# Kernel tuning notes

Measured on AMD Instinct MI355X. Metric: run time of the kernel, lower is better.

The kernel has to match this reference:

```python
import jax, jax.numpy as jnp
import numpy as np

JITTER = 1e-6
LOG_2PI_BASE = 2.0 * np.pi  # multiplied by sigma_sq inside log


def rbf_kernel(x1, x2, lengthscale, outputscale):
    """gpytorch ScaleKernel(RBFKernel): outputscale * exp(-0.5 * ||(x1-x2)/ls||^2)."""
    x1s = x1 / lengthscale
    x2s = x2 / lengthscale
    sq = (jnp.sum(x1s * x1s, axis=1)[:, None]
          + jnp.sum(x2s * x2s, axis=1)[None, :]
          - 2.0 * (x1s @ x2s.T))
    sq = jnp.maximum(sq, 0.0)
    return outputscale * jnp.exp(-0.5 * sq)


def setup_inputs() -> dict:
    key = jax.random.key(0)
    k = jax.random.split(key, 4)
    n, m, d = 8192, 512, 8
    return {
        "train_x": jax.random.normal(k[0], (n, d), dtype=jnp.float32),
        "train_y": jax.random.normal(k[1], (n,), dtype=jnp.float32),
        "inducing_points": jax.random.normal(k[2], (m, d), dtype=jnp.float32),
        "q_mu": jnp.zeros((m, 1), dtype=jnp.float32),
        "q_log_var": jnp.eye(m, dtype=jnp.float32),
        "likelihood_log_variance": jnp.asarray(0.0, dtype=jnp.float32),
        "lengthscale": jnp.asarray(1.0, dtype=jnp.float32),
        "outputscale": jnp.asarray(1.0, dtype=jnp.float32),
    }


def reference(train_x, train_y, inducing_points, q_mu, q_log_var,
              likelihood_log_variance, lengthscale, outputscale):
    n = train_x.shape[0]
    m = inducing_points.shape[0]
    eye_m = jnp.eye(m, dtype=train_x.dtype)

    # --- predict(train_x): q(f) = N(pred_mean, pred_cov) ---
    K_ff = rbf_kernel(train_x, train_x, lengthscale, outputscale)          # [n, n]
    K_uu = rbf_kernel(inducing_points, inducing_points, lengthscale, outputscale) + JITTER * eye_m
    K_uf = rbf_kernel(inducing_points, train_x, lengthscale, outputscale)  # [m, n]

    L_uu = jnp.linalg.cholesky(K_uu)                                       # lower [m, m]
    Lam = jax.scipy.linalg.solve_triangular(L_uu, K_uf, lower=True)        # [m, n]
    pred_mean = (Lam.T @ q_mu)[:, 0]                                       # [n]

    q_sqrt = jnp.tril(jnp.exp(0.5 * q_log_var))                            # [m, m]
    q_cov = q_sqrt @ q_sqrt.T + JITTER * eye_m                             # [m, m]

    S = K_ff - Lam.T @ Lam                                                 # [n, n]
    V = Lam.T @ q_cov                                                      # [n, m]
    pred_cov = S + V @ V.T                                                 # [n, n]

    # --- expected log likelihood E_{q(f)}[log N(y | f, sigma^2 I)] / n ---
    sigma_sq = jnp.exp(likelihood_log_variance)
    diff = train_y - pred_mean
    ell = jnp.sum(-0.5 * (diff * diff + jnp.diagonal(pred_cov)) / sigma_sq
                  - 0.5 * jnp.log(LOG_2PI_BASE * sigma_sq)) / n

    # --- KL( N(q_mu, q_cov) || N(0, I) ) / n ---
    Lq = jnp.linalg.cholesky(q_cov)
    logdet_q = 2.0 * jnp.sum(jnp.log(jnp.diagonal(Lq)))
    mu = q_mu[:, 0]
    kl = 0.5 * (jnp.trace(q_cov) + mu @ mu - m - logdet_q) / n

    return ell - kl
```

## Files before the change

### kernel.cpp

```cpp
#include <hip/hip_runtime.h>
#include <math.h>

#define MI 512
#define NPT 8192
#define JIT 1e-6f
#define LOG2PI 1.8378770664093453f

#define OFF_A     0
#define OFF_LINV  262144
#define OFF_QS    524288
#define OFF_QC    786432
#define OFF_DINV  1048576
#define OFF_PART  1081856
#define OFF_FLAGS 1082368
#define NFLAGS 211

#define FMA16(ACC,a0,a1,a2,a3,b0,b1,b2,b3) \
  ACC[0][0]+=a0*b0; ACC[0][1]+=a0*b1; ACC[0][2]+=a0*b2; ACC[0][3]+=a0*b3; \
  ACC[1][0]+=a1*b0; ACC[1][1]+=a1*b1; ACC[1][2]+=a1*b2; ACC[1][3]+=a1*b3; \
  ACC[2][0]+=a2*b0; ACC[2][1]+=a2*b1; ACC[2][2]+=a2*b2; ACC[2][3]+=a2*b3; \
  ACC[3][0]+=a3*b0; ACC[3][1]+=a3*b1; ACC[3][2]+=a3*b2; ACC[3][3]+=a3*b3;

typedef float f4 __attribute__((ext_vector_type(4)));

__device__ __forceinline__ f4 ld_coh(const float* p) {
  f4 r;
  asm volatile("global_load_dwordx4 %0, %1, off sc0 sc1\n\ts_waitcnt vmcnt(0)"
               : "=v"(r) : "v"(p) : "memory");
  return r;
}
__device__ __forceinline__ void ld_coh4x4(const float* p0, const float* p1,
    const float* p2, const float* p3, f4& a, f4& b, f4& c, f4& d) {
  asm volatile(
    "global_load_dwordx4 %0, %4, off sc0 sc1\n\t"
    "global_load_dwordx4 %1, %5, off sc0 sc1\n\t"
    "global_load_dwordx4 %2, %6, off sc0 sc1\n\t"
    "global_load_dwordx4 %3, %7, off sc0 sc1\n\t"
    "s_waitcnt vmcnt(0)"
    : "=&v"(a), "=&v"(b), "=&v"(c), "=&v"(d)
    : "v"(p0), "v"(p1), "v"(p2), "v"(p3) : "memory");
}
__device__ __forceinline__ void st_coh(float* p, f4 v) {
  asm volatile("global_store_dwordx4 %0, %1, off sc0 sc1" :: "v"(p), "v"(v) : "memory");
}

__device__ __forceinline__ void wait_flag(unsigned* f, int tid) {
  if (tid == 0) {
    while (__hip_atomic_load(f, __ATOMIC_RELAXED, __HIP_MEMORY_SCOPE_AGENT) == 0)
      __builtin_amdgcn_s_sleep(2);
    __builtin_amdgcn_fence(__ATOMIC_ACQUIRE, "agent");
  }
  __syncthreads();
}
__device__ __forceinline__ void wait_count(unsigned* c, unsigned tgt, int tid) {
  if (tid == 0) {
    while (__hip_atomic_load(c, __ATOMIC_RELAXED, __HIP_MEMORY_SCOPE_AGENT) < tgt)
      __builtin_amdgcn_s_sleep(2);
    __builtin_amdgcn_fence(__ATOMIC_ACQUIRE, "agent");
  }
  __syncthreads();
}
__device__ __forceinline__ void publish_tile(unsigned* f, unsigned* cnt, int tid) {
  __syncthreads();
  if (tid == 0) {
    __builtin_amdgcn_fence(__ATOMIC_RELEASE, "agent");
    __hip_atomic_store(f, 1u, __ATOMIC_RELAXED, __HIP_MEMORY_SCOPE_AGENT);
    __hip_atomic_fetch_add(cnt, 1u, __ATOMIC_RELAXED, __HIP_MEMORY_SCOPE_AGENT);
  }
}
__device__ __forceinline__ void wait_flag_nf(unsigned* f, int tid) {
  if (tid == 0)
    while (__hip_atomic_load(f, __ATOMIC_RELAXED, __HIP_MEMORY_SCOPE_AGENT) == 0)
      __builtin_amdgcn_s_sleep(2);
  __syncthreads();
}
__device__ __forceinline__ void raise_flag_nf(unsigned* f, int tid) {
  asm volatile("s_waitcnt vmcnt(0)" ::: "memory");
  __syncthreads();
  if (tid == 0)
    __hip_atomic_store(f, 1u, __ATOMIC_RELAXED, __HIP_MEMORY_SCOPE_AGENT);
}

#define SCAT65(Sdst, fi, gv) { int r_=(fi)>>4, c_=((fi)&15)*4; \
  Sdst[r_*65+c_+0]=gv.x; Sdst[r_*65+c_+1]=gv.y; Sdst[r_*65+c_+2]=gv.z; Sdst[r_*65+c_+3]=gv.w; }

__global__ __launch_bounds__(256) void k_prep(const float* __restrict__ Z,
    const float* __restrict__ qlv, const float* __restrict__ lsP,
    const float* __restrict__ osP, float* __restrict__ ws) {
  int u = blockIdx.x*256 + threadIdx.x;
  if (blockIdx.x < 27) {
    int fi = blockIdx.x*256 + threadIdx.x;
    if (fi < NFLAGS*32) ((unsigned*)(ws + OFF_FLAGS))[fi] = 0u;
  }
  float ls = lsP[0], os = osP[0];
  float ils2 = 1.0f/(ls*ls);
  if (u < MI*MI) {
    int i = u >> 9, j = u & 511;
    float4 a0 = *(const float4*)(Z + i*8);
    float4 a1 = *(const float4*)(Z + i*8 + 4);
    float4 b0 = *(const float4*)(Z + j*8);
    float4 b1 = *(const float4*)(Z + j*8 + 4);
    float d0=a0.x-b0.x, d1=a0.y-b0.y, d2=a0.z-b0.z, d3=a0.w-b0.w;
    float d4=a1.x-b1.x, d5=a1.y-b1.y, d6=a1.z-b1.z, d7=a1.w-b1.w;
    float sq = d0*d0+d1*d1+d2*d2+d3*d3+d4*d4+d5*d5+d6*d6+d7*d7;
    float v = os*__expf(-0.5f*ils2*sq);
    if (i==j) v += JIT;
    ws[OFF_A + u] = v;
  } else {
    int w2 = u - MI*MI;
    if (w2 < MI*MI) {
      int i = w2 >> 9, j = w2 & 511;
      ws[OFF_QS + w2] = (j <= i) ? __expf(0.5f*qlv[w2]) : 0.0f;
    }
  }
}

__global__ __launch_bounds__(256, 3) void k_dag(const float* __restrict__ X,
    const float* __restrict__ Yv, const float* __restrict__ Z,
    const float* __restrict__ qmu, const float* __restrict__ qlv,
    const float* __restrict__ llvP, const float* __restrict__ lsP,
    const float* __restrict__ osP, float* __restrict__ ws,
    float* __restrict__ out) {
  __shared__ float SH[13340];
  float* A    = ws + OFF_A;
  float* LT   = ws + OFF_LINV;
  const float* QC = ws + OFF_QC;
  float* DINV = ws + OFF_DINV;
  float* PART = ws + OFF_PART;
  unsigned* FB = (unsigned*)(ws + OFF_FLAGS);
  #define FLA(i) (FB + (i)*32)
  int bid = blockIdx.x, tid = threadIdx.x;
  int ty4 = (tid >> 4)*4, tx4 = (tid & 15)*4;

  if (bid < 8) {
    __builtin_amdgcn_s_setprio(3);
    int b = bid, Rb = b*64;
    float* Dg = SH;
    float* Sa = SH + 4160;
    float* Sb = SH + 8320;
    float* TMP = SH + 12480;
    for (int e = tid; e < 4096; e += 256)
      Dg[(e>>6)*65 + (e&63)] = A[(Rb + (e>>6))*512 + Rb + (e&63)];

    for (int p = 0; p < b; ++p) {
      if (p > 0) wait_flag_nf(FLA(144 + b*8 + p), tid);
      {
        int f0 = tid, f1 = tid+256, f2 = tid+512, f3 = tid+768;
        f4 g0,g1,g2,g3;
        ld_coh4x4(A + (Rb + (f0>>4))*512 + p*64 + (f0&15)*4,
                  A + (Rb + (f1>>4))*512 + p*64 + (f1&15)*4,
                  A + (Rb + (f2>>4))*512 + p*64 + (f2&15)*4,
                  A + (Rb + (f3>>4))*512 + p*64 + (f3&15)*4, g0,g1,g2,g3);
        SCAT65(Sb, f0, g0) SCAT65(Sb, f1, g1) SCAT65(Sb, f2, g2) SCAT65(Sb, f3, g3)
      }
      wait_flag_nf(FLA(p), tid);
      {
        int f0 = tid, f1 = tid+256, f2 = tid+512, f3 = tid+768;
        f4 d0,d1,d2,d3;
        ld_coh4x4(DINV + p*4096 + f0*4, DINV + p*4096 + f1*4,
                  DINV + p*4096 + f2*4, DINV + p*4096 + f3*4, d0,d1,d2,d3);
        SCAT65(Sa, f0, d0) SCAT65(Sa, f1, d1) SCAT65(Sa, f2, d2) SCAT65(Sa, f3, d3)
      }
      __syncthreads();
      float acc2[4][4] = {{0.f}};
      for (int m = 0; m < 64; ++m) {
        float a0=Sb[(ty4+0)*65+m],a1=Sb[(ty4+1)*65+m],a2=Sb[(ty4+2)*65+m],a3=Sb[(ty4+3)*65+m];
        float b0=Sa[(tx4+0)*65+m],b1=Sa[(tx4+1)*65+m],b2=Sa[(tx4+2)*65+m],b3=Sa[(tx4+3)*65+m];
        FMA16(acc2,a0,a1,a2,a3,b0,b1,b2,b3)
      }
      __syncthreads();
      #pragma unroll
      for (int u = 0; u < 4; ++u) {
        f4 lv = {acc2[u][0], acc2[u][1], acc2[u][2], acc2[u][3]};
        st_coh(A + (Rb+ty4+u)*512 + p*64 + tx4, lv);
        Sb[(ty4+u)*65 + tx4+0] = acc2[u][0];
        Sb[(ty4+u)*65 + tx4+1] = acc2[u][1];
        Sb[(ty4+u)*65 + tx4+2] = acc2[u][2];
        Sb[(ty4+u)*65 + tx4+3] = acc2[u][3];
      }
      raise_flag_nf(FLA(8 + b*8 + p), tid);
      float c2[4][4] = {{0.f}};
      for (int m = 0; m < 64; ++m) {
        float a0=Sb[(ty4+0)*65+m],a1=Sb[(ty4+1)*65+m],a2=Sb[(ty4+2)*65+m],a3=Sb[(ty4+3)*65+m];
        float b0=Sb[(tx4+0)*65+m],b1=Sb[(tx4+1)*65+m],b2=Sb[(tx4+2)*65+m],b3=Sb[(tx4+3)*65+m];
        FMA16(c2,a0,a1,a2,a3,b0,b1,b2,b3)
      }
      #pragma unroll
      for (int u = 0; u < 4; ++u)
        #pragma unroll
        for (int v = 0; v < 4; ++v)
          Dg[(ty4+u)*65 + tx4+v] -= c2[u][v];
    }
    __syncthreads();

    for (int e = tid; e < 4096; e += 256) Sa[(e>>6)*65 + (e&63)] = 0.0f;
    __syncthreads();
    for (int t = 0; t < 4; ++t) {
      const int c0 = t*16;
      if (tid < 16) {
        float a[16];
        #pragma unroll
        for (int j = 0; j < 16; ++j) a[j] = Dg[(c0+tid)*65 + c0 + j];
        float rr = 0.f;
        #pragma unroll
        for (int j = 0; j < 16; ++j) {
          float d = __shfl(a[j], j);
          float r = rsqrtf(d);
          r = r*(1.5f - 0.5f*d*r*r);
          if (tid == j) rr = r;
          a[j] *= r;
          #pragma unroll
          for (int k = j+1; k < 16; ++k)
            a[k] -= a[j]*__shfl(a[j], k);
        }
        #pragma unroll
        for (int j = 0; j < 16; ++j)
          Dg[(c0+tid)*65 + c0 + j] = (j <= tid) ? a[j] : 0.0f;
        float v[16];
        #pragma unroll
        for (int i = 0; i < 16; ++i) {
          float s = (tid == i) ? 1.0f : 0.0f;
          #pragma unroll
          for (int k = 0; k < i; ++k)
            s -= Dg[(c0+i)*65 + c0 + k]*v[k];
          v[i] = s * __shfl(rr, i);
        }
        #pragma unroll
        for (int i = 0; i < 16; ++i)
          Sa[(c0+i)*65 + c0 + tid] = v[i];
      }
      __syncthreads();
      if (t < 3) {
        const int cnt = 48 - c0;
        const int r0 = c0 + 16;
        float res[3];
        int nout = cnt*16, idx = 0;
        for (int e = tid; e < nout; e += 256, ++idx) {
          int r = r0 + (e >> 4), j = e & 15;
          float s = 0.f;
          #pragma unroll
          for (int m = 0; m < 16; ++m)
            s += Dg[r*65 + c0 + m]*Sa[(c0+j)*65 + c0 + m];
          res[idx] = s;
        }
        __syncthreads();
        idx = 0;
        for (int e = tid; e < nout; e += 256, ++idx)
          Dg[(r0 + (e >> 4))*65 + c0 + (e & 15)] = res[idx];
        __syncthreads();
        for (int e = tid; e < cnt*cnt; e += 256) {
          int r = r0 + e/cnt, c = r0 + e%cnt;
          float s = 0.f;
          #pragma unroll
          for (int m = 0; m < 16; ++m)
            s += Dg[r*65 + c0 + m]*Dg[c*65 + c0 + m];
          Dg[r*65 + c] -= s;
        }
        __syncthreads();
      }
    }
    for (int d = 1; d < 4; ++d) {
      int nout = (4-d)*256;
      for (int e = tid; e < nout; e += 256) {
        int bs = e >> 8, I = bs, J = I + d;
        int i = (e >> 4) & 15, c = e & 15;
        float s = 0.f;
        for (int k = I; k < J; ++k) {
          #pragma unroll
          for (int m = 0; m < 16; ++m)
            s += Dg[(J*16+i)*65 + k*16+m]*Sa[(k*16+m)*65 + I*16+c];
        }
        TMP[bs*272 + i*17 + c] = s;
      }
      __syncthreads();
      for (int e = tid; e < nout; e += 256) {
        int bs = e >> 8, I = bs, J = I + d;
        int i = (e >> 4) & 15, c = e & 15;
        float s = 0.f;
        #pragma unroll
        for (int m = 0; m < 16; ++m)
          s += Sa[(J*16+i)*65 + J*16+m]*TMP[bs*272 + m*17 + c];
        Sa[(J*16+i)*65 + I*16+c] = -s;
      }
      __syncthreads();
    }
    #pragma unroll
    for (int kk = 0; kk < 4; ++kk) {
      int fi = tid + kk*256; int r_ = fi>>4, c_ = (fi&15)*4;
      f4 dv = {Sa[r_*65+c_+0], Sa[r_*65+c_+1], Sa[r_*65+c_+2], Sa[r_*65+c_+3]};
      st_coh(DINV + b*4096 + fi*4, dv);
    }
    raise_flag_nf(FLA(b), tid);
    return;
  }

  if (bid < 44) {
    __builtin_amdgcn_s_setprio(2);
    int t = bid - 8;
    int s = 0, rem = t;
    while (rem >= s+1) { rem -= (s+1); ++s; }
    int J = rem;
    if (s == J) {
      wait_flag_nf(FLA(s), tid);
      {
        int f0 = tid, f1 = tid+256, f2 = tid+512, f3 = tid+768;
        f4 d0,d1,d2,d3;
        ld_coh4x4(DINV + s*4096 + f0*4, DINV + s*4096 + f1*4,
                  DINV + s*4096 + f2*4, DINV + s*4096 + f3*4, d0,d1,d2,d3);
        #define LTW(fi, dv) { int i_=(fi)>>4, j_=((fi)&15)*4; \
          LT[(64*s+j_+0)*512+64*s+i_]=dv.x; LT[(64*s+j_+1)*512+64*s+i_]=dv.y; \
          LT[(64*s+j_+2)*512+64*s+i_]=dv.z; LT[(64*s+j_+3)*512+64*s+i_]=dv.w; }
        LTW(f0, d0) LTW(f1, d1) LTW(f2, d2) LTW(f3, d3)
      }
      publish_tile(FLA(72 + s*8 + J), FLA(136 + s), tid);
      return;
    }
    float* Ls = SH;
    float* Vs = SH + 4160;
    float* T  = SH + 8320;
    float acc[4][4] = {{0.f}};
    for (int k = J; k < s; ++k) {
      wait_flag(FLA(72 + k*8 + J), tid);
      wait_flag_nf(FLA(8 + s*8 + k), tid);
      {
        int f0 = tid, f1 = tid+256, f2 = tid+512, f3 = tid+768;
        f4 a0,a1,a2,a3;
        ld_coh4x4(A + (64*s+(f0>>4))*512 + 64*k + (f0&15)*4,
                  A + (64*s+(f1>>4))*512 + 64*k + (f1&15)*4,
                  A + (64*s+(f2>>4))*512 + 64*k + (f2&15)*4,
                  A + (64*s+(f3>>4))*512 + 64*k + (f3&15)*4, a0,a1,a2,a3);
        #define LSV(fi, av) { int row=(fi)>>4, m4=((fi)&15)*4; \
          Ls[row*65+m4+0]=av.x; Ls[row*65+m4+1]=av.y; Ls[row*65+m4+2]=av.z; Ls[row*65+m4+3]=av.w; \
          float4 v = *(const float4*)(LT + (64*J+row)*512 + 64*k + m4); \
          Vs[(m4+0)*65+row]=v.x; Vs[(m4+1)*65+row]=v.y; Vs[(m4+2)*65+row]=v.z; Vs[(m4+3)*65+row]=v.w; }
        LSV(f0, a0) LSV(f1, a1) LSV(f2, a2) LSV(f3, a3)
      }
      __syncthreads();
      for (int m = 0; m < 64; ++m) {
        float a0=Ls[(ty4+0)*65+m],a1=Ls[(ty4+1)*65+m],a2=Ls[(ty4+2)*65+m],a3=Ls[(ty4+3)*65+m];
        float b0=Vs[m*65+tx4+0],b1=Vs[m*65+tx4+1],b2=Vs[m*65+tx4+2],b3=Vs[m*65+tx4+3];
        FMA16(acc,a0,a1,a2,a3,b0,b1,b2,b3)
      }
      __syncthreads();
    }
    wait_flag_nf(FLA(s), tid);
    #pragma unroll
    for (int u = 0; u < 4; ++u)
      #pragma unroll
      for (int v = 0; v < 4; ++v)
        T[(ty4+u)*65 + tx4+v] = acc[u][v];
    {
      int f0 = tid, f1 = tid+256, f2 = tid+512, f3 = tid+768;
      f4 d0,d1,d2,d3;
      ld_coh4x4(DINV + s*4096 + f0*4, DINV + s*4096 + f1*4,
                DINV + s*4096 + f2*4, DINV + s*4096 + f3*4, d0,d1,d2,d3);
      SCAT65(Ls, f0, d0) SCAT65(Ls, f1, d1) SCAT65(Ls, f2, d2) SCAT65(Ls, f3, d3)
    }
    __syncthreads();
    float acc2[4][4] = {{0.f}};
    for (int m = 0; m < 64; ++m) {
      float a0=Ls[(ty4+0)*65+m],a1=Ls[(ty4+1)*65+m],a2=Ls[(ty4+2)*65+m],a3=Ls[(ty4+3)*65+m];
      float b0=T[m*65+tx4+0],b1=T[m*65+tx4+1],b2=T[m*65+tx4+2],b3=T[m*65+tx4+3];
      FMA16(acc2,a0,a1,a2,a3,b0,b1,b2,b3)
    }
    #pragma unroll
    for (int u = 0; u < 4; ++u)
      #pragma unroll
      for (int v = 0; v < 4; ++v)
        LT[(64*J+tx4+v)*512 + 64*s+ty4+u] = -acc2[u][v];
    publish_tile(FLA(72 + s*8 + J), FLA(136 + s), tid);
    return;
  }

  if (bid < 65) {
    __builtin_amdgcn_s_setprio(2);
    int hid = bid - 44;
    int b = 2, rem = hid;
    while (rem >= b-1) { rem -= (b-1); ++b; }
    int p = rem + 1;
    float* Sa = SH;
    float* Sb = SH + 4160;
    float gacc[4][4] = {{0.f}};
    for (int pp = 0; pp < p; ++pp) {
      wait_flag_nf(FLA(8 + b*8 + pp), tid);
      wait_flag_nf(FLA(8 + p*8 + pp), tid);
      {
        int f0 = tid, f1 = tid+256, f2 = tid+512, f3 = tid+768;
        f4 a0,a1,a2,a3, b0,b1,b2,b3;
        ld_coh4x4(A + (b*64+(f0>>4))*512 + pp*64 + (f0&15)*4,
                  A + (b*64+(f1>>4))*512 + pp*64 + (f1&15)*4,
                  A + (b*64+(f2>>4))*512 + pp*64 + (f2&15)*4,
                  A + (b*64+(f3>>4))*512 + pp*64 + (f3&15)*4, a0,a1,a2,a3);
        ld_coh4x4(A + (p*64+(f0>>4))*512 + pp*64 + (f0&15)*4,
                  A + (p*64+(f1>>4))*512 + pp*64 + (f1&15)*4,
                  A + (p*64+(f2>>4))*512 + pp*64 + (f2&15)*4,
                  A + (p*64+(f3>>4))*512 + pp*64 + (f3&15)*4, b0,b1,b2,b3);
        SCAT65(Sa, f0, a0) SCAT65(Sa, f1, a1) SCAT65(Sa, f2, a2) SCAT65(Sa, f3, a3)
        SCAT65(Sb, f0, b0) SCAT65(Sb, f1, b1) SCAT65(Sb, f2, b2) SCAT65(Sb, f3, b3)
      }
      __syncthreads();
      for (int m = 0; m < 64; ++m) {
        float a0=Sa[(ty4+0)*65+m],a1=Sa[(ty4+1)*65+m],a2=Sa[(ty4+2)*65+m],a3=Sa[(ty4+3)*65+m];
        float b0=Sb[(tx4+0)*65+m],b1=Sb[(tx4+1)*65+m],b2=Sb[(tx4+2)*65+m],b3=Sb[(tx4+3)*65+m];
        FMA16(gacc,a0,a1,a2,a3,b0,b1,b2,b3)
      }
      __syncthreads();
    }
    {
      float* r0 = A + (b*64+ty4+0)*512 + p*64 + tx4;
      float* r1 = A + (b*64+ty4+1)*512 + p*64 + tx4;
      float* r2 = A + (b*64+ty4+2)*512 + p*64 + tx4;
      float* r3 = A + (b*64+ty4+3)*512 + p*64 + tx4;
      f4 o0,o1,o2,o3;
      ld_coh4x4(r0, r1, r2, r3, o0,o1,o2,o3);
      f4 n0 = {o0.x-gacc[0][0], o0.y-gacc[0][1], o0.z-gacc[0][2], o0.w-gacc[0][3]};
      f4 n1 = {o1.x-gacc[1][0], o1.y-gacc[1][1], o1.z-gacc[1][2], o1.w-gacc[1][3]};
      f4 n2 = {o2.x-gacc[2][0], o2.y-gacc[2][1], o2.z-gacc[2][2], o2.w-gacc[2][3]};
      f4 n3 = {o3.x-gacc[3][0], o3.y-gacc[3][1], o3.z-gacc[3][2], o3.w-gacc[3][3]};
      st_coh(r0, n0); st_coh(r1, n1); st_coh(r2, n2); st_coh(r3, n3);
    }
    raise_flag_nf(FLA(144 + b*8 + p), tid);
    return;
  }

  if (bid < 129) {
    __builtin_amdgcn_s_setprio(1);
    int cid = bid - 65;
    int bi = cid >> 3, bj = cid & 7;
    const float* QSp = ws + OFF_QS;
    float* QCw = ws + OFF_QC;
    float* Xs2 = SH;
    float* Ys2 = SH + 1280;
    int lrow = tid >> 2, lc4 = (tid & 3)*4;
    float acc[4][4] = {{0.f}};
    for (int kc = 0; kc < 512; kc += 16) {
      float4 xa = *(const float4*)(QSp + (bi*64+lrow)*512 + kc + lc4);
      float4 ya = *(const float4*)(QSp + (bj*64+lrow)*512 + kc + lc4);
      Xs2[lrow*20+lc4+0]=xa.x; Xs2[lrow*20+lc4+1]=xa.y; Xs2[lrow*20+lc4+2]=xa.z; Xs2[lrow*20+lc4+3]=xa.w;
      Ys2[lrow*20+lc4+0]=ya.x; Ys2[lrow*20+lc4+1]=ya.y; Ys2[lrow*20+lc4+2]=ya.z; Ys2[lrow*20+lc4+3]=ya.w;
      __syncthreads();
      #pragma unroll
      for (int kk = 0; kk < 16; ++kk) {
        float a0=Xs2[(ty4+0)*20+kk],a1=Xs2[(ty4+1)*20+kk],a2=Xs2[(ty4+2)*20+kk],a3=Xs2[(ty4+3)*20+kk];
        float b0=Ys2[(tx4+0)*20+kk],b1=Ys2[(tx4+1)*20+kk],b2=Ys2[(tx4+2)*20+kk],b3=Ys2[(tx4+3)*20+kk];
        FMA16(acc,a0,a1,a2,a3,b0,b1,b2,b3)
      }
      __syncthreads();
    }
    #pragma unroll
    for (int u = 0; u < 4; ++u)
      #pragma unroll
      for (int v = 0; v < 4; ++v) {
        int gi = bi*64+ty4+u, gj = bj*64+tx4+v;
        float o = acc[u][v]; if (gi==gj) o += JIT;
        QCw[gi*512+gj] = o;
      }
    __syncthreads();
    if (tid == 0) {
      __builtin_amdgcn_fence(__ATOMIC_RELEASE, "agent");
      __hip_atomic_fetch_add(FLA(208), 1u, __ATOMIC_RELAXED, __HIP_MEMORY_SCOPE_AGENT);
    }
    return;
  }

  {
    int B = bid - 129;
    float* KL  = SH;
    float* PB  = SH + 8192;
    float* FB2 = SH + 11456;
    float* qsh = SH + 12736;
    float* Xs  = SH + 8192;
    float* RD  = SH + 8192;
    float* elli= SH + 9824;
    int* lastf = (int*)(SH + 13248);
    float ls = lsP[0], os = osP[0], llv = llvP[0];
    float ils2 = 1.0f/(ls*ls);
    if (tid < 128) { int pp = tid>>3, d = tid&7; Xs[pp*8+d] = X[(B*16+pp)*8 + d]; }
    qsh[tid] = qmu[tid]; qsh[tid+256] = qmu[tid+256];
    __syncthreads();
    for (int e = tid; e < 8192; e += 256) {
      int cc = e >> 4, pp = e & 15;
      float4 z0 = *(const float4*)(Z + cc*8);
      float4 z1 = *(const float4*)(Z + cc*8 + 4);
      float d0=z0.x-Xs[pp*8+0], d1=z0.y-Xs[pp*8+1], d2=z0.z-Xs[pp*8+2], d3=z0.w-Xs[pp*8+3];
      float d4=z1.x-Xs[pp*8+4], d5=z1.y-Xs[pp*8+5], d6=z1.z-Xs[pp*8+6], d7=z1.w-Xs[pp*8+7];
      float sq = d0*d0+d1*d1+d2*d2+d3*d3+d4*d4+d5*d5+d6*d6+d7*d7;
      KL[e] = os*__expf(-0.5f*ils2*sq);
    }
    wait_count(FLA(208), 64u, tid);

    int gq = tid >> 6;
    int lr = (tid >> 2) & 15;
    int lrow4 = lr*4;
    int pq4 = (tid & 3)*4;
    int rq4 = (tid >> 2)*4;
    float pmp[4] = {0.f,0.f,0.f,0.f}, lsp[4] = {0.f,0.f,0.f,0.f};
    float ua0[4][4] = {{0.f}}, ua1[4][4] = {{0.f}};

    for (int s = 0; s < 8; ++s) {
      wait_count(FLA(136 + s), (unsigned)(s+1), tid);
      int Q = 16*(s+1);
      int cbeg = gq*Q, cend = cbeg + Q;
      float acc[4][4] = {{0.f}};
      const float* Lcol = LT + 64*s + lrow4;
      #pragma unroll 4
      for (int c = cbeg; c < cend; ++c) {
        float4 kv = *(const float4*)&KL[c*16 + pq4];
        float4 lv = *(const float4*)(Lcol + c*512);
        FMA16(acc, lv.x,lv.y,lv.z,lv.w, kv.x,kv.y,kv.z,kv.w)
      }
      if (gq > 0) {
        float* pb = PB + (gq-1)*1088;
        #pragma unroll
        for (int u = 0; u < 4; ++u)
          #pragma unroll
          for (int v = 0; v < 4; ++v)
            pb[(lrow4+u)*17 + pq4+v] = acc[u][v];
      }
      __syncthreads();
      if (gq == 0) {
        #pragma unroll
        for (int u = 0; u < 4; ++u) {
          float qv = qsh[64*s + lrow4 + u];
          #pragma unroll
          for (int v = 0; v < 4; ++v) {
            float f = acc[u][v]
                    + PB[(lrow4+u)*17 + pq4+v]
                    + PB[1088 + (lrow4+u)*17 + pq4+v]
                    + PB[2176 + (lrow4+u)*17 + pq4+v];
            FB2[(lrow4+u)*20 + pq4+v] = f;
            pmp[v] += f*qv;
            lsp[v] += f*f;
          }
        }
      }
      __syncthreads();
      #pragma unroll 2
      for (int cl = 0; cl < 64; ++cl) {
        float4 kv = *(const float4*)&FB2[cl*20 + pq4];
        float4 q0 = *(const float4*)(QC + (64*s+cl)*512 + rq4);
        float4 q1 = *(const float4*)(QC + (64*s+cl)*512 + 256 + rq4);
        FMA16(ua0, q0.x,q0.y,q0.z,q0.w, kv.x,kv.y,kv.z,kv.w)
        FMA16(ua1, q1.x,q1.y,q1.z,q1.w, kv.x,kv.y,kv.z,kv.w)
      }
    }
    __syncthreads();

    if (gq == 0) {
      #pragma unroll
      for (int v = 0; v < 4; ++v) {
        RD[lr*17 + pq4+v] = pmp[v];
        RD[272 + lr*17 + pq4+v] = lsp[v];
      }
    }
    float usq[4] = {0.f,0.f,0.f,0.f};
    #pragma unroll
    for (int u = 0; u < 4; ++u)
      #pragma unroll
      for (int v = 0; v < 4; ++v)
        usq[v] += ua0[u][v]*ua0[u][v] + ua1[u][v]*ua1[u][v];
    #pragma unroll
    for (int v = 0; v < 4; ++v)
      RD[544 + (tid>>2)*17 + pq4+v] = usq[v];
    __syncthreads();
    if (tid < 16) {
      float pm = 0.f, lq = 0.f, us = 0.f;
      for (int r2 = 0; r2 < 16; ++r2) {
        pm += RD[r2*17 + tid];
        lq += RD[272 + r2*17 + tid];
      }
      for (int r2 = 0; r2 < 64; ++r2)
        us += RD[544 + r2*17 + tid];
      int gi = B*16 + tid;
      float diff = Yv[gi] - pm;
      float diagc = os + us - lq;
      float iss = __expf(-llv);
      elli[tid] = -0.5f*((diff*diff + diagc)*iss + (LOG2PI + llv));
    }
    __syncthreads();
    if (tid == 0) {
      float sum = 0.f;
      #pragma unroll
      for (int i2 = 0; i2 < 16; ++i2) sum += elli[i2];
      PART[B] = sum;
      __builtin_amdgcn_fence(__ATOMIC_RELEASE, "agent");
      unsigned old = __hip_atomic_fetch_add(FLA(209), 1u, __ATOMIC_RELAXED, __HIP_MEMORY_SCOPE_AGENT);
      lastf[0] = (old == 511u) ? 1 : 0;
    }
    __syncthreads();
    if (lastf[0]) {
      if (tid == 0) __builtin_amdgcn_fence(__ATOMIC_ACQUIRE, "agent");
      __syncthreads();
      double* sh = (double*)SH;
      double pa = 0.0, tr = 0.0, mm = 0.0, ld = 0.0;
      for (int i = tid; i < 512; i += 256) {
        pa += (double)PART[i];
        tr += (double)QC[i*513];
        double q = (double)qmu[i]; mm += q*q;
        ld += (double)qlv[i*513];
      }
      double vals[4] = {pa, tr, mm, ld};
      double res[4];
      for (int t2 = 0; t2 < 4; ++t2) {
        sh[tid] = vals[t2]; __syncthreads();
        for (int s2 = 128; s2 > 0; s2 >>= 1) {
          if (tid < s2) sh[tid] += sh[tid+s2];
          __syncthreads();
        }
        res[t2] = sh[0]; __syncthreads();
      }
      if (tid == 0) {
        double n = 8192.0;
        double ell = res[0]/n;
        double kl = 0.5*(res[1] + res[2] - 512.0 - res[3])/n;
        out[0] = (float)(ell - kl);
      }
    }
  }
}

extern "C" void kernel_launch(void* const* d_in, const int* in_sizes, int n_in,
                              void* d_out, int out_size, void* d_ws, size_t ws_size,
                              hipStream_t stream) {
  (void)in_sizes; (void)n_in; (void)out_size; (void)ws_size;
  const float* X   = (const float*)d_in[0];
  const float* Y   = (const float*)d_in[1];
  const float* Z   = (const float*)d_in[2];
  const float* qmu = (const float*)d_in[3];
  const float* qlv = (const float*)d_in[4];
  const float* llv = (const float*)d_in[5];
  const float* ls  = (const float*)d_in[6];
  const float* os  = (const float*)d_in[7];
  float* ws = (float*)d_ws;
  float* out = (float*)d_out;

  k_prep<<<2048, 256, 0, stream>>>(Z, qlv, ls, os, ws);
  k_dag<<<641, 256, 0, stream>>>(X, Y, Z, qmu, qlv, llv, ls, os, ws, out);
}
```

Before: 344.8 us.

## Publish diagonal inverse in 16-column chunks to pipeline Cholesky critical path

The diagonal-block Cholesky workers now compute the inverse of each 16x16 sub-block row incrementally and publish each 16-row slice of DINV with its own flag. For the sub-diagonal panel p=b-1, the next diagonal block consumes these slices as they arrive, computing the panel TRSM and SYRK update in 16-column pieces. The goal is to shorten the serial critical path across the diagonal blocks. The cost is 33 extra flags, more syncthreads, finer-grained waits, and a separate code path for the last panel.

```diff
diff --git a/kernel.cpp b/kernel.cpp
--- a/kernel.cpp
+++ b/kernel.cpp
@@ -13,7 +13,7 @@
 #define OFF_DINV  1048576
 #define OFF_PART  1081856
 #define OFF_FLAGS 1082368
-#define NFLAGS 211
+#define NFLAGS 244
 
 #define FMA16(ACC,a0,a1,a2,a3,b0,b1,b2,b3) \
   ACC[0][0]+=a0*b0; ACC[0][1]+=a0*b1; ACC[0][2]+=a0*b2; ACC[0][3]+=a0*b3; \
@@ -88,7 +88,7 @@
     const float* __restrict__ qlv, const float* __restrict__ lsP,
     const float* __restrict__ osP, float* __restrict__ ws) {
   int u = blockIdx.x*256 + threadIdx.x;
-  if (blockIdx.x < 27) {
+  if (blockIdx.x < 31) {
     int fi = blockIdx.x*256 + threadIdx.x;
     if (fi < NFLAGS*32) ((unsigned*)(ws + OFF_FLAGS))[fi] = 0u;
   }
@@ -121,7 +121,7 @@
     const float* __restrict__ llvP, const float* __restrict__ lsP,
     const float* __restrict__ osP, float* __restrict__ ws,
     float* __restrict__ out) {
-  __shared__ float SH[13340];
+  __shared__ float SH[13568];
   float* A    = ws + OFF_A;
   float* LT   = ws + OFF_LINV;
   const float* QC = ws + OFF_QC;
@@ -138,11 +138,11 @@
     float* Dg = SH;
     float* Sa = SH + 4160;
     float* Sb = SH + 8320;
-    float* TMP = SH + 12480;
+    float* Sq = SH + 12480;
     for (int e = tid; e < 4096; e += 256)
       Dg[(e>>6)*65 + (e&63)] = A[(Rb + (e>>6))*512 + Rb + (e&63)];
 
-    for (int p = 0; p < b; ++p) {
+    for (int p = 0; p < b-1; ++p) {
       if (p > 0) wait_flag_nf(FLA(144 + b*8 + p), tid);
       {
         int f0 = tid, f1 = tid+256, f2 = tid+512, f3 = tid+768;
@@ -191,6 +191,61 @@
         for (int v = 0; v < 4; ++v)
           Dg[(ty4+u)*65 + tx4+v] -= c2[u][v];
     }
+
+    if (b > 0) {
+      int p = b - 1;
+      if (p > 0) wait_flag_nf(FLA(144 + b*8 + p), tid);
+      {
+        int f0 = tid, f1 = tid+256, f2 = tid+512, f3 = tid+768;
+        f4 g0,g1,g2,g3;
+        ld_coh4x4(A + (Rb + (f0>>4))*512 + p*64 + (f0&15)*4,
+                  A + (Rb + (f1>>4))*512 + p*64 + (f1&15)*4,
+                  A + (Rb + (f2>>4))*512 + p*64 + (f2&15)*4,
+                  A + (Rb + (f3>>4))*512 + p*64 + (f3&15)*4, g0,g1,g2,g3);
+        SCAT65(Sb, f0, g0) SCAT65(Sb, f1, g1) SCAT65(Sb, f2, g2) SCAT65(Sb, f3, g3)
+      }
+      float c2[4][4] = {{0.f}};
+      int qi = tid >> 2, qj4 = (tid & 3)*4;
+      for (int q = 0; q < 4; ++q) {
+        wait_flag_nf(FLA(212 + p*4 + q), tid);
+        {
+          int r = tid >> 4, c4 = (tid & 15)*4;
+          f4 d = ld_coh(DINV + p*4096 + (16*q + r)*64 + c4);
+          Sa[(16*q + r)*65 + c4+0] = d.x; Sa[(16*q + r)*65 + c4+1] = d.y;
+          Sa[(16*q + r)*65 + c4+2] = d.z; Sa[(16*q + r)*65 + c4+3] = d.w;
+        }
+        __syncthreads();
+        float o0=0.f, o1=0.f, o2=0.f, o3=0.f;
+        for (int m = 0; m < 64; ++m) {
+          float g = Sb[qi*65 + m];
+          o0 += g*Sa[(16*q+qj4+0)*65+m];
+          o1 += g*Sa[(16*q+qj4+1)*65+m];
+          o2 += g*Sa[(16*q+qj4+2)*65+m];
+          o3 += g*Sa[(16*q+qj4+3)*65+m];
+        }
+        f4 ov = {o0, o1, o2, o3};
+        st_coh(A + (Rb+qi)*512 + p*64 + 16*q + qj4, ov);
+        Sq[qi*17 + qj4+0] = o0; Sq[qi*17 + qj4+1] = o1;
+        Sq[qi*17 + qj4+2] = o2; Sq[qi*17 + qj4+3] = o3;
+        __syncthreads();
+        #pragma unroll
+        for (int u = 0; u < 4; ++u)
+          #pragma unroll
+          for (int v = 0; v < 4; ++v) {
+            float s = 0.f;
+            #pragma unroll
+            for (int m = 0; m < 16; ++m)
+              s += Sq[(ty4+u)*17+m]*Sq[(tx4+v)*17+m];
+            c2[u][v] += s;
+          }
+      }
+      raise_flag_nf(FLA(8 + b*8 + p), tid);
+      #pragma unroll
+      for (int u = 0; u < 4; ++u)
+        #pragma unroll
+        for (int v = 0; v < 4; ++v)
+          Dg[(ty4+u)*65 + tx4+v] -= c2[u][v];
+    }
     __syncthreads();
 
     for (int e = tid; e < 4096; e += 256) Sa[(e>>6)*65 + (e&63)] = 0.0f;
@@ -230,6 +285,35 @@
           Sa[(c0+i)*65 + c0 + tid] = v[i];
       }
       __syncthreads();
+      for (int I = t-1; I >= 0; --I) {
+        {
+          int i = tid >> 4, c = tid & 15;
+          float s = 0.f;
+          for (int k = I; k < t; ++k) {
+            #pragma unroll
+            for (int m = 0; m < 16; ++m)
+              s += Dg[(c0+i)*65 + k*16+m] * Sa[(k*16+m)*65 + I*16+c];
+          }
+          Sq[i*17 + c] = s;
+        }
+        __syncthreads();
+        {
+          int i = tid >> 4, c = tid & 15;
+          float s = 0.f;
+          #pragma unroll
+          for (int m = 0; m < 16; ++m)
+            s += Sa[(c0+i)*65 + c0+m] * Sq[m*17 + c];
+          Sa[(c0+i)*65 + I*16+c] = -s;
+        }
+        __syncthreads();
+      }
+      {
+        int r = tid >> 4, c4 = (tid & 15)*4;
+        f4 dv = {Sa[(c0+r)*65+c4+0], Sa[(c0+r)*65+c4+1],
+                 Sa[(c0+r)*65+c4+2], Sa[(c0+r)*65+c4+3]};
+        st_coh(DINV + b*4096 + (c0+r)*64 + c4, dv);
+      }
+      raise_flag_nf(FLA(212 + b*4 + t), tid);
       if (t < 3) {
         const int cnt = 48 - c0;
         const int r0 = c0 + 16;
@@ -258,37 +342,6 @@
         }
         __syncthreads();
       }
-    }
-    for (int d = 1; d < 4; ++d) {
-      int nout = (4-d)*256;
-      for (int e = tid; e < nout; e += 256) {
-        int bs = e >> 8, I = bs, J = I + d;
-        int i = (e >> 4) & 15, c = e & 15;
-        float s = 0.f;
-        for (int k = I; k < J; ++k) {
-          #pragma unroll
-          for (int m = 0; m < 16; ++m)
-            s += Dg[(J*16+i)*65 + k*16+m]*Sa[(k*16+m)*65 + I*16+c];
-        }
-        TMP[bs*272 + i*17 + c] = s;
-      }
-      __syncthreads();
-      for (int e = tid; e < nout; e += 256) {
-        int bs = e >> 8, I = bs, J = I + d;
-        int i = (e >> 4) & 15, c = e & 15;
-        float s = 0.f;
-        #pragma unroll
-        for (int m = 0; m < 16; ++m)
-          s += Sa[(J*16+i)*65 + J*16+m]*TMP[bs*272 + m*17 + c];
-        Sa[(J*16+i)*65 + I*16+c] = -s;
-      }
-      __syncthreads();
-    }
-    #pragma unroll
-    for (int kk = 0; kk < 4; ++kk) {
-      int fi = tid + kk*256; int r_ = fi>>4, c_ = (fi&15)*4;
-      f4 dv = {Sa[r_*65+c_+0], Sa[r_*65+c_+1], Sa[r_*65+c_+2], Sa[r_*65+c_+3]};
-      st_coh(DINV + b*4096 + fi*4, dv);
     }
     raise_flag_nf(FLA(b), tid);
     return;
@@ -472,7 +525,7 @@
     float* Xs  = SH + 8192;
     float* RD  = SH + 8192;
     float* elli= SH + 9824;
-    int* lastf = (int*)(SH + 13248);
+    int* lastf = (int*)(SH + 13264);
     float ls = lsP[0], os = osP[0], llv = llvP[0];
     float ils2 = 1.0f/(ls*ls);
     if (tid < 128) { int pp = tid>>3, d = tid&7; Xs[pp*8+d] = X[(B*16+pp)*8 + d]; }
```

New measurement: 420.7 us. 22.0% more time.

## Compute K_uu tiles on the fly inside the DAG kernel instead of prep

Applied to the files above, without the earlier changes.

The prep kernel no longer materialises the full 512x512 K_uu matrix. The Cholesky diagonal blocks, the first panel and the Schur-update blocks now evaluate RBF entries directly from the inducing points when they need them. This removes a global write and reread of the kernel matrix and halves the prep grid. The cost is recomputing the exponential in the dependency-critical blocks. The spin-wait sleep interval is also shortened to react faster to flags.

```diff
diff --git a/kernel.cpp b/kernel.cpp
--- a/kernel.cpp
+++ b/kernel.cpp
@@ -22,6 +22,16 @@
   ACC[3][0]+=a3*b0; ACC[3][1]+=a3*b1; ACC[3][2]+=a3*b2; ACC[3][3]+=a3*b3;
 
 typedef float f4 __attribute__((ext_vector_type(4)));
+
+#define RBF8(ZI, ZJ, OUT) { \
+  float4 ra0 = *(const float4*)(Z + (ZI)*8); \
+  float4 ra1 = *(const float4*)(Z + (ZI)*8 + 4); \
+  float4 rb0 = *(const float4*)(Z + (ZJ)*8); \
+  float4 rb1 = *(const float4*)(Z + (ZJ)*8 + 4); \
+  float e0=ra0.x-rb0.x, e1=ra0.y-rb0.y, e2=ra0.z-rb0.z, e3=ra0.w-rb0.w; \
+  float e4=ra1.x-rb1.x, e5=ra1.y-rb1.y, e6=ra1.z-rb1.z, e7=ra1.w-rb1.w; \
+  float rsq = e0*e0+e1*e1+e2*e2+e3*e3+e4*e4+e5*e5+e6*e6+e7*e7; \
+  OUT = os*__expf(-0.5f*ils2*rsq); }
 
 __device__ __forceinline__ f4 ld_coh(const float* p) {
   f4 r;
@@ -71,7 +81,7 @@
 __device__ __forceinline__ void wait_flag_nf(unsigned* f, int tid) {
   if (tid == 0)
     while (__hip_atomic_load(f, __ATOMIC_RELAXED, __HIP_MEMORY_SCOPE_AGENT) == 0)
-      __builtin_amdgcn_s_sleep(2);
+      __builtin_amdgcn_s_sleep(1);
   __syncthreads();
 }
 __device__ __forceinline__ void raise_flag_nf(unsigned* f, int tid) {
@@ -84,34 +94,15 @@
 #define SCAT65(Sdst, fi, gv) { int r_=(fi)>>4, c_=((fi)&15)*4; \
   Sdst[r_*65+c_+0]=gv.x; Sdst[r_*65+c_+1]=gv.y; Sdst[r_*65+c_+2]=gv.z; Sdst[r_*65+c_+3]=gv.w; }
 
-__global__ __launch_bounds__(256) void k_prep(const float* __restrict__ Z,
-    const float* __restrict__ qlv, const float* __restrict__ lsP,
-    const float* __restrict__ osP, float* __restrict__ ws) {
+__global__ __launch_bounds__(256) void k_prep(const float* __restrict__ qlv,
+    float* __restrict__ ws) {
   int u = blockIdx.x*256 + threadIdx.x;
-  if (blockIdx.x < 27) {
-    int fi = blockIdx.x*256 + threadIdx.x;
-    if (fi < NFLAGS*32) ((unsigned*)(ws + OFF_FLAGS))[fi] = 0u;
-  }
-  float ls = lsP[0], os = osP[0];
-  float ils2 = 1.0f/(ls*ls);
+  if (blockIdx.x < 31) {
+    if (u < NFLAGS*32) ((unsigned*)(ws + OFF_FLAGS))[u] = 0u;
+  }
   if (u < MI*MI) {
     int i = u >> 9, j = u & 511;
-    float4 a0 = *(const float4*)(Z + i*8);
-    float4 a1 = *(const float4*)(Z + i*8 + 4);
-    float4 b0 = *(const float4*)(Z + j*8);
-    float4 b1 = *(const float4*)(Z + j*8 + 4);
-    float d0=a0.x-b0.x, d1=a0.y-b0.y, d2=a0.z-b0.z, d3=a0.w-b0.w;
-    float d4=a1.x-b1.x, d5=a1.y-b1.y, d6=a1.z-b1.z, d7=a1.w-b1.w;
-    float sq = d0*d0+d1*d1+d2*d2+d3*d3+d4*d4+d5*d5+d6*d6+d7*d7;
-    float v = os*__expf(-0.5f*ils2*sq);
-    if (i==j) v += JIT;
-    ws[OFF_A + u] = v;
-  } else {
-    int w2 = u - MI*MI;
-    if (w2 < MI*MI) {
-      int i = w2 >> 9, j = w2 & 511;
-      ws[OFF_QS + w2] = (j <= i) ? __expf(0.5f*qlv[w2]) : 0.0f;
-    }
+    ws[OFF_QS + u] = (j <= i) ? __expf(0.5f*qlv[u]) : 0.0f;
   }
 }
 
@@ -135,16 +126,22 @@
   if (bid < 8) {
     __builtin_amdgcn_s_setprio(3);
     int b = bid, Rb = b*64;
+    float ls = lsP[0], os = osP[0];
+    float ils2 = 1.0f/(ls*ls);
     float* Dg = SH;
     float* Sa = SH + 4160;
     float* Sb = SH + 8320;
     float* TMP = SH + 12480;
-    for (int e = tid; e < 4096; e += 256)
-      Dg[(e>>6)*65 + (e&63)] = A[(Rb + (e>>6))*512 + Rb + (e&63)];
+    for (int e = tid; e < 4096; e += 256) {
+      int i = e>>6, j = e&63;
+      float v; RBF8(Rb+i, Rb+j, v);
+      if (i==j) v += JIT;
+      Dg[i*65 + j] = v;
+    }
 
     for (int p = 0; p < b; ++p) {
-      if (p > 0) wait_flag_nf(FLA(144 + b*8 + p), tid);
-      {
+      if (p > 0) {
+        wait_flag_nf(FLA(144 + b*8 + p), tid);
         int f0 = tid, f1 = tid+256, f2 = tid+512, f3 = tid+768;
         f4 g0,g1,g2,g3;
         ld_coh4x4(A + (Rb + (f0>>4))*512 + p*64 + (f0&15)*4,
@@ -152,6 +149,12 @@
                   A + (Rb + (f2>>4))*512 + p*64 + (f2&15)*4,
                   A + (Rb + (f3>>4))*512 + p*64 + (f3&15)*4, g0,g1,g2,g3);
         SCAT65(Sb, f0, g0) SCAT65(Sb, f1, g1) SCAT65(Sb, f2, g2) SCAT65(Sb, f3, g3)
+      } else {
+        for (int e = tid; e < 4096; e += 256) {
+          int i = e>>6, j = e&63;
+          float v; RBF8(Rb+i, j, v);
+          Sb[i*65 + j] = v;
+        }
       }
       wait_flag_nf(FLA(p), tid);
       {
@@ -378,6 +381,8 @@
     int b = 2, rem = hid;
     while (rem >= b-1) { rem -= (b-1); ++b; }
     int p = rem + 1;
+    float ls = lsP[0], os = osP[0];
+    float ils2 = 1.0f/(ls*ls);
     float* Sa = SH;
     float* Sb = SH + 4160;
     float gacc[4][4] = {{0.f}};
@@ -406,18 +411,15 @@
       }
       __syncthreads();
     }
-    {
-      float* r0 = A + (b*64+ty4+0)*512 + p*64 + tx4;
-      float* r1 = A + (b*64+ty4+1)*512 + p*64 + tx4;
-      float* r2 = A + (b*64+ty4+2)*512 + p*64 + tx4;
-      float* r3 = A + (b*64+ty4+3)*512 + p*64 + tx4;
-      f4 o0,o1,o2,o3;
-      ld_coh4x4(r0, r1, r2, r3, o0,o1,o2,o3);
-      f4 n0 = {o0.x-gacc[0][0], o0.y-gacc[0][1], o0.z-gacc[0][2], o0.w-gacc[0][3]};
-      f4 n1 = {o1.x-gacc[1][0], o1.y-gacc[1][1], o1.z-gacc[1][2], o1.w-gacc[1][3]};
-      f4 n2 = {o2.x-gacc[2][0], o2.y-gacc[2][1], o2.z-gacc[2][2], o2.w-gacc[2][3]};
-      f4 n3 = {o3.x-gacc[3][0], o3.y-gacc[3][1], o3.z-gacc[3][2], o3.w-gacc[3][3]};
-      st_coh(r0, n0); st_coh(r1, n1); st_coh(r2, n2); st_coh(r3, n3);
+    #pragma unroll
+    for (int u = 0; u < 4; ++u) {
+      float v0,v1,v2,v3;
+      RBF8(b*64+ty4+u, p*64+tx4+0, v0);
+      RBF8(b*64+ty4+u, p*64+tx4+1, v1);
+      RBF8(b*64+ty4+u, p*64+tx4+2, v2);
+      RBF8(b*64+ty4+u, p*64+tx4+3, v3);
+      f4 nv = {v0-gacc[u][0], v1-gacc[u][1], v2-gacc[u][2], v3-gacc[u][3]};
+      st_coh(A + (b*64+ty4+u)*512 + p*64 + tx4, nv);
     }
     raise_flag_nf(FLA(144 + b*8 + p), tid);
     return;
@@ -634,6 +636,6 @@
   float* ws = (float*)d_ws;
   float* out = (float*)d_out;
 
-  k_prep<<<2048, 256, 0, stream>>>(Z, qlv, ls, os, ws);
+  k_prep<<<1024, 256, 0, stream>>>(qlv, ws);
   k_dag<<<641, 256, 0, stream>>>(X, Y, Z, qmu, qlv, llv, ls, os, ws, out);
 }
```

Measured after the change: 346.1 us, median of 2. About the same (+0.4%).
